# Optimization experiments

Measured on AMD Instinct MI355X. Metric: run time of the kernel, lower is better.

Reference implementation:

```python
import jax, jax.numpy as jnp
import numpy as np

B = 4096
IN_FEATS = 1024
OUT_FEATS = 1024
NUM_HEADS = 16
NUM_MEMS = 4096
HEAD_DIM = OUT_FEATS // NUM_HEADS
TEMPERATURE = 1.0
EPS = 0.0  # original code uses plain jnp.linalg.norm (no eps)


def setup_inputs() -> dict:
    key = jax.random.key(0)
    k1, k2, k3 = jax.random.split(key, 3)
    x = jax.random.normal(k1, (B, IN_FEATS), dtype=jnp.float32)
    # eqx.nn.Linear stores weight as [out, in]; uniform-like init replaced with normal scaled
    W_q = jax.random.normal(k2, (OUT_FEATS, IN_FEATS), dtype=jnp.float32) * (1.0 / np.sqrt(IN_FEATS))
    memories = jax.random.normal(k3, (NUM_HEADS, NUM_MEMS, HEAD_DIM), dtype=jnp.float32) * 0.02
    return {"x": x, "W_q": W_q, "memories": memories}


def reference(x, W_q, memories):
    # q = query_proj(x): [B, out_feats] -> [B, H, d]
    q = (x @ W_q.T).reshape(B, NUM_HEADS, HEAD_DIM)
    # L2-normalize queries and memories along feature dim
    q_norm = q / jnp.linalg.norm(q, axis=-1, keepdims=True)
    mem_norm = memories / jnp.linalg.norm(memories, axis=-1, keepdims=True)
    # cosine-similarity scores: [B, H, M]
    attn_scores = jnp.einsum('bhd,hmd->bhm', q_norm, mem_norm)
    # soft readout (hard=False branch)
    mem_probs = jax.nn.softmax(attn_scores / TEMPERATURE, axis=-1)
    # weighted combine of normalized memories, scaled by sqrt(head_dim)
    out = jnp.einsum('bhm,hmd->bhd', mem_probs, mem_norm) * jnp.sqrt(HEAD_DIM).astype(x.dtype)
    return out.reshape(B, OUT_FEATS)
```

## Files before the change

kernel.cpp:

```cpp
#include <hip/hip_runtime.h>
#include <stdint.h>

#define B_SZ  4096
#define HEADS 16
#define HD    64
#define M_SZ  4096
#define K_IN  1024
#define SW    72
#define LOG2E 1.44269504088896f

typedef _Float16 f16;
typedef f16  f16x4 __attribute__((ext_vector_type(4)));
typedef f16  f16x8 __attribute__((ext_vector_type(8)));
typedef float f32x4 __attribute__((ext_vector_type(4)));

union U8 { uint4 u4; f16x8 h8; unsigned int ui[4]; unsigned short us[8]; };

__device__ __forceinline__ unsigned short f2h(float f) {
    _Float16 h = (_Float16)f;
    return __builtin_bit_cast(unsigned short, h);
}
__device__ __forceinline__ f16x8 ldsv8(const unsigned short* p) {
    U8 u; u.u4 = *reinterpret_cast<const uint4*>(p); return u.h8;
}

#if __has_builtin(__builtin_amdgcn_exp2f)
#define EXP2F(x) __builtin_amdgcn_exp2f(x)
#else
#define EXP2F(x) __expf((x) * 0.6931471805599453f)
#endif

__device__ __forceinline__ void gload_lds16(const void* g, void* l) {
    __builtin_amdgcn_global_load_lds(
        (const __attribute__((address_space(1))) void*)g,
        (__attribute__((address_space(3))) void*)l, 16, 0, 0);
}

__global__ __launch_bounds__(256) void k_conv(const float* __restrict__ x,
                                              const float* __restrict__ Wq,
                                              unsigned short* __restrict__ xh,
                                              unsigned short* __restrict__ Wh) {
    const int b = blockIdx.x;
    const float* src;
    unsigned short* dst;
    size_t base;
    if (b < 2048) { src = x;  dst = xh; base = (size_t)b * 2048; }
    else          { src = Wq; dst = Wh; base = (size_t)(b - 2048) * 2048; }
    const size_t i = base + (size_t)threadIdx.x * 8;
    float4 f0 = reinterpret_cast<const float4*>(src + i)[0];
    float4 f1 = reinterpret_cast<const float4*>(src + i)[1];
    U8 u;
    u.us[0] = f2h(f0.x); u.us[1] = f2h(f0.y); u.us[2] = f2h(f0.z); u.us[3] = f2h(f0.w);
    u.us[4] = f2h(f1.x); u.us[5] = f2h(f1.y); u.us[6] = f2h(f1.z); u.us[7] = f2h(f1.w);
    *reinterpret_cast<uint4*>(dst + i) = u.u4;
}

__global__ __launch_bounds__(256) void k_prep_mem(const float* __restrict__ mem,
                                                  unsigned short* __restrict__ F) {
    __shared__ float part[64][4];
    __shared__ float scale[64];
    __shared__ unsigned short Tn[64 * SW];

    const int h  = blockIdx.y;
    const int tl = blockIdx.x;
    const int m0 = tl * 64;
    const int tid = threadIdx.x;
    const int r = tid >> 2;
    const int c = tid & 3;

    const float* src = mem + ((size_t)(h * M_SZ + m0 + r)) * HD + c * 16;
    float v[16];
    float ss = 0.f;
#pragma unroll
    for (int i = 0; i < 4; i++) {
        float4 f = reinterpret_cast<const float4*>(src)[i];
        v[4*i+0] = f.x; v[4*i+1] = f.y; v[4*i+2] = f.z; v[4*i+3] = f.w;
        ss += f.x*f.x + f.y*f.y + f.z*f.z + f.w*f.w;
    }
    part[r][c] = ss;
    __syncthreads();
    if (tid < 64) {
        float s = part[tid][0] + part[tid][1] + part[tid][2] + part[tid][3];
        scale[tid] = rsqrtf(s);
    }
    __syncthreads();
    const float sc = scale[r];

    U8 a, b;
#pragma unroll
    for (int i = 0; i < 8; i++) { a.us[i] = f2h(v[i] * sc); b.us[i] = f2h(v[8 + i] * sc); }
    *reinterpret_cast<uint4*>(&Tn[r * SW + c * 16])     = a.u4;
    *reinterpret_cast<uint4*>(&Tn[r * SW + c * 16 + 8]) = b.u4;
    __syncthreads();

    const int w = tid >> 6, lane = tid & 63;
    const int l15 = lane & 15, quad = lane >> 4;
    unsigned short* Fd = F + ((size_t)(h * 64 + tl) * 16) * 512;

#pragma unroll
    for (int i = 0; i < 2; i++) {
        const int ch = w * 2 + i, g = ch >> 1, s = ch & 1;
        const int mp = 32 * (g >> 1) + ((l15 >> 2) * 8) + 4 * (g & 1) + (l15 & 3);
        uint4 vv = *reinterpret_cast<const uint4*>(&Tn[mp * SW + s * 32 + quad * 8]);
        *reinterpret_cast<uint4*>(Fd + ch * 512 + lane * 8) = vv;
    }
#pragma unroll
    for (int i = 0; i < 2; i++) {
        const int c2 = w * 2 + i, p = c2 >> 2, n = c2 & 3;
        U8 u;
#pragma unroll
        for (int j = 0; j < 8; j++)
            u.us[j] = Tn[(32 * p + quad * 8 + j) * SW + n * 16 + l15];
        *reinterpret_cast<uint4*>(Fd + (8 + c2) * 512 + lane * 8) = u.u4;
    }
}

__global__ __launch_bounds__(256, 2) void k_qproj(const unsigned short* __restrict__ xh,
                                                  const unsigned short* __restrict__ Wh,
                                                  unsigned short* __restrict__ qn) {
    __shared__ unsigned short As[128 * SW];
    __shared__ unsigned short Bs[64 * SW];

    const int b0 = blockIdx.x * 128;
    const int n0 = blockIdx.y * 64;
    const int t = threadIdx.x;
    const int w = t >> 6, lane = t & 63;
    const int l15 = lane & 15, quad = lane >> 4;

    f32x4 acc[2][4] = {};

    for (int kb = 0; kb < K_IN; kb += 64) {
        __syncthreads();
        {
            const unsigned short* px = xh + (size_t)(b0 + (t >> 1)) * K_IN + kb + (t & 1) * 32;
            const unsigned short* pw = Wh + (size_t)(n0 + (t >> 2)) * K_IN + kb + (t & 3) * 16;
            uint4 av[4];
#pragma unroll
            for (int i = 0; i < 4; i++) av[i] = reinterpret_cast<const uint4*>(px)[i];
            uint4 bv[2];
#pragma unroll
            for (int i = 0; i < 2; i++) bv[i] = reinterpret_cast<const uint4*>(pw)[i];
#pragma unroll
            for (int i = 0; i < 4; i++)
                *reinterpret_cast<uint4*>(&As[(t >> 1) * SW + (t & 1) * 32 + i * 8]) = av[i];
#pragma unroll
            for (int i = 0; i < 2; i++)
                *reinterpret_cast<uint4*>(&Bs[(t >> 2) * SW + (t & 3) * 16 + i * 8]) = bv[i];
        }
        __syncthreads();

#pragma unroll
        for (int s = 0; s < 2; s++) {
            f16x8 af[2];
#pragma unroll
            for (int qg = 0; qg < 2; qg++)
                af[qg] = ldsv8(&As[(w * 32 + qg * 16 + l15) * SW + s * 32 + quad * 8]);
#pragma unroll
            for (int g = 0; g < 4; g++) {
                f16x8 bf_ = ldsv8(&Bs[(g * 16 + l15) * SW + s * 32 + quad * 8]);
#pragma unroll
                for (int qg = 0; qg < 2; qg++)
                    acc[qg][g] = __builtin_amdgcn_mfma_f32_16x16x32_f16(af[qg], bf_, acc[qg][g], 0, 0, 0);
            }
        }
    }

    __syncthreads();
    unsigned short* Ct = As;
#pragma unroll
    for (int qg = 0; qg < 2; qg++) {
        float ssq[4];
#pragma unroll
        for (int r = 0; r < 4; r++) {
            float s = 0.f;
#pragma unroll
            for (int g = 0; g < 4; g++) s += acc[qg][g][r] * acc[qg][g][r];
            ssq[r] = s;
        }
#pragma unroll
        for (int mask = 1; mask <= 8; mask <<= 1)
#pragma unroll
            for (int r = 0; r < 4; r++) ssq[r] += __shfl_xor(ssq[r], mask, 64);
#pragma unroll
        for (int r = 0; r < 4; r++) {
            float inv = rsqrtf(ssq[r]) * LOG2E;
#pragma unroll
            for (int g = 0; g < 4; g++)
                Ct[(w * 32 + qg * 16 + quad * 4 + r) * SW + g * 16 + l15] = f2h(acc[qg][g][r] * inv);
        }
    }
    __syncthreads();

    const int row = t >> 1, half = (t & 1) * 32;
    unsigned short* dq = qn + (size_t)(b0 + row) * 1024 + n0 + half;
#pragma unroll
    for (int i = 0; i < 4; i++)
        reinterpret_cast<uint4*>(dq)[i] = *reinterpret_cast<const uint4*>(&Ct[row * SW + half + i * 8]);
}

__global__ __launch_bounds__(256, 2) void k_attn(const unsigned short* __restrict__ qn,
                                                 const unsigned short* __restrict__ F,
                                                 float* __restrict__ out) {
    __shared__ unsigned short buf[2][8192];

    const int b = blockIdx.x;
    const int h  = 2 * (b & 7) + (b >> 8);
    const int b0 = ((b >> 3) & 31) * 128;
    const int t = threadIdx.x;
    const int w = t >> 6, lane = t & 63;
    const int l15 = lane & 15, quad = lane >> 4;

    f16x8 qf[2][2];
#pragma unroll
    for (int qg = 0; qg < 2; qg++)
#pragma unroll
        for (int s = 0; s < 2; s++) {
            U8 u;
            u.u4 = *reinterpret_cast<const uint4*>(
                qn + (size_t)(b0 + w * 32 + qg * 16 + l15) * 1024 + h * 64 + s * 32 + quad * 8);
            qf[qg][s] = u.h8;
        }

    const unsigned short* Fh = F + (size_t)h * 64 * 8192;

#pragma unroll
    for (int i = 0; i < 4; i++) {
        const int ch = w * 4 + i;
        gload_lds16(Fh + ch * 512 + lane * 8, &buf[0][ch * 512]);
    }

    f32x4 accO[2][4] = {};
    float lsum[2] = {0.f, 0.f};

    for (int tl = 0; tl < 64; ++tl) {
        __syncthreads();
        const int cur = tl & 1;

        if (tl + 1 < 64) {
            const unsigned short* gn = Fh + (size_t)(tl + 1) * 8192;
#pragma unroll
            for (int i = 0; i < 4; i++) {
                const int ch = w * 4 + i;
                gload_lds16(gn + ch * 512 + lane * 8, &buf[cur ^ 1][ch * 512]);
            }
        }

        const unsigned short* lb = buf[cur];
        f16x8 am[8], bw[8];
#pragma unroll
        for (int ch = 0; ch < 8; ch++) am[ch] = ldsv8(&lb[ch * 512 + lane * 8]);
#pragma unroll
        for (int ch = 0; ch < 8; ch++) bw[ch] = ldsv8(&lb[(8 + ch) * 512 + lane * 8]);

#pragma unroll
        for (int qg = 0; qg < 2; qg++) {
#pragma unroll
            for (int p = 0; p < 2; p++) {
                f32x4 s0 = {0.f, 0.f, 0.f, 0.f}, s1 = {0.f, 0.f, 0.f, 0.f};
                s0 = __builtin_amdgcn_mfma_f32_16x16x32_f16(am[4*p+0], qf[qg][0], s0, 0, 0, 0);
                s0 = __builtin_amdgcn_mfma_f32_16x16x32_f16(am[4*p+1], qf[qg][1], s0, 0, 0, 0);
                s1 = __builtin_amdgcn_mfma_f32_16x16x32_f16(am[4*p+2], qf[qg][0], s1, 0, 0, 0);
                s1 = __builtin_amdgcn_mfma_f32_16x16x32_f16(am[4*p+3], qf[qg][1], s1, 0, 0, 0);

                float p0 = EXP2F(s0[0]), p1 = EXP2F(s0[1]), p2 = EXP2F(s0[2]), p3 = EXP2F(s0[3]);
                float p4 = EXP2F(s1[0]), p5 = EXP2F(s1[1]), p6 = EXP2F(s1[2]), p7 = EXP2F(s1[3]);
                lsum[qg] += ((p0 + p1) + (p2 + p3)) + ((p4 + p5) + (p6 + p7));

                U8 pu;
#if __has_builtin(__builtin_amdgcn_cvt_pkrtz)
                pu.ui[0] = __builtin_bit_cast(unsigned int, __builtin_amdgcn_cvt_pkrtz(p0, p1));
                pu.ui[1] = __builtin_bit_cast(unsigned int, __builtin_amdgcn_cvt_pkrtz(p2, p3));
                pu.ui[2] = __builtin_bit_cast(unsigned int, __builtin_amdgcn_cvt_pkrtz(p4, p5));
                pu.ui[3] = __builtin_bit_cast(unsigned int, __builtin_amdgcn_cvt_pkrtz(p6, p7));
#else
                pu.us[0]=f2h(p0); pu.us[1]=f2h(p1); pu.us[2]=f2h(p2); pu.us[3]=f2h(p3);
                pu.us[4]=f2h(p4); pu.us[5]=f2h(p5); pu.us[6]=f2h(p6); pu.us[7]=f2h(p7);
#endif
#pragma unroll
                for (int n = 0; n < 4; n++)
                    accO[qg][n] = __builtin_amdgcn_mfma_f32_16x16x32_f16(pu.h8, bw[p * 4 + n], accO[qg][n], 0, 0, 0);
            }
        }
    }

#pragma unroll
    for (int qg = 0; qg < 2; qg++) {
        float s = lsum[qg];
        s += __shfl_xor(s, 16, 64);
        s += __shfl_xor(s, 32, 64);
        float inv = 8.0f / s;
#pragma unroll
        for (int r = 0; r < 4; r++) {
            float iv = __shfl(inv, quad * 4 + r, 64);
            float* po = out + (size_t)(b0 + w * 32 + qg * 16 + quad * 4 + r) * 1024 + h * 64;
#pragma unroll
            for (int n = 0; n < 4; n++)
                po[n * 16 + l15] = accO[qg][n][r] * iv;
        }
    }
}

extern "C" void kernel_launch(void* const* d_in, const int* in_sizes, int n_in,
                              void* d_out, int out_size, void* d_ws, size_t ws_size,
                              hipStream_t stream) {
    (void)in_sizes; (void)n_in; (void)out_size; (void)ws_size;
    const float* x   = (const float*)d_in[0];
    const float* Wq  = (const float*)d_in[1];
    const float* mem = (const float*)d_in[2];
    float* out = (float*)d_out;

    unsigned short* qn = (unsigned short*)d_ws;
    unsigned short* F  = qn + (size_t)B_SZ * 1024;
    unsigned short* xh = F  + (size_t)HEADS * 64 * 16 * 512;
    unsigned short* Wh = xh + (size_t)B_SZ * K_IN;

    k_conv    <<<2560, 256, 0, stream>>>(x, Wq, xh, Wh);
    k_prep_mem<<<dim3(64, 16), 256, 0, stream>>>(mem, F);
    k_qproj   <<<dim3(32, 16), 256, 0, stream>>>(xh, Wh, qn);
    k_attn    <<<512, 256, 0, stream>>>(qn, F, out);
}
```

Baseline: 179.1 us.

## Fuse fp32-to-fp16 conversion into q-projection GEMM and double attention tile size

Drops the separate conversion kernel: the q-projection now reads fp32 x and W_q directly and converts to fp16 while staging tiles into shared memory. The projection tile grows to 128x128 (two heads per block) with 256 blocks. The attention kernel now processes two memory tiles per iteration with a larger double buffer and a scheduling barrier. This removes one launch and the round-trip of fp16 copies through memory. In exchange it doubles the fp32 global reads per tile, gives less parallelism in the GEMM, and raises LDS and register pressure in the attention kernel, which may reduce occupancy.

```diff
diff --git a/kernel.cpp b/kernel.cpp
--- a/kernel.cpp
+++ b/kernel.cpp
@@ -30,29 +30,16 @@
 #define EXP2F(x) __expf((x) * 0.6931471805599453f)
 #endif
 
+#if __has_builtin(__builtin_amdgcn_sched_barrier)
+#define SCHED_FENCE() __builtin_amdgcn_sched_barrier(0)
+#else
+#define SCHED_FENCE()
+#endif
+
 __device__ __forceinline__ void gload_lds16(const void* g, void* l) {
     __builtin_amdgcn_global_load_lds(
         (const __attribute__((address_space(1))) void*)g,
         (__attribute__((address_space(3))) void*)l, 16, 0, 0);
-}
-
-__global__ __launch_bounds__(256) void k_conv(const float* __restrict__ x,
-                                              const float* __restrict__ Wq,
-                                              unsigned short* __restrict__ xh,
-                                              unsigned short* __restrict__ Wh) {
-    const int b = blockIdx.x;
-    const float* src;
-    unsigned short* dst;
-    size_t base;
-    if (b < 2048) { src = x;  dst = xh; base = (size_t)b * 2048; }
-    else          { src = Wq; dst = Wh; base = (size_t)(b - 2048) * 2048; }
-    const size_t i = base + (size_t)threadIdx.x * 8;
-    float4 f0 = reinterpret_cast<const float4*>(src + i)[0];
-    float4 f1 = reinterpret_cast<const float4*>(src + i)[1];
-    U8 u;
-    u.us[0] = f2h(f0.x); u.us[1] = f2h(f0.y); u.us[2] = f2h(f0.z); u.us[3] = f2h(f0.w);
-    u.us[4] = f2h(f1.x); u.us[5] = f2h(f1.y); u.us[6] = f2h(f1.z); u.us[7] = f2h(f1.w);
-    *reinterpret_cast<uint4*>(dst + i) = u.u4;
 }
 
 __global__ __launch_bounds__(256) void k_prep_mem(const float* __restrict__ mem,
@@ -115,37 +102,49 @@
     }
 }
 
-__global__ __launch_bounds__(256, 2) void k_qproj(const unsigned short* __restrict__ xh,
-                                                  const unsigned short* __restrict__ Wh,
-                                                  unsigned short* __restrict__ qn) {
-    __shared__ unsigned short As[128 * SW];
-    __shared__ unsigned short Bs[64 * SW];
-
-    const int b0 = blockIdx.x * 128;
-    const int n0 = blockIdx.y * 64;
+__global__ __launch_bounds__(256) void k_qproj(const float* __restrict__ x,
+                                               const float* __restrict__ Wq,
+                                               unsigned short* __restrict__ qn) {
+    __shared__ unsigned short sbuf[2 * 128 * SW];
+    unsigned short* As = sbuf;
+    unsigned short* Bs = sbuf + 128 * SW;
+
+    const int bx = blockIdx.x;
+    const int n0 = (bx & 7) * 128;
+    const int b0 = (bx >> 3) * 128;
     const int t = threadIdx.x;
     const int w = t >> 6, lane = t & 63;
     const int l15 = lane & 15, quad = lane >> 4;
 
-    f32x4 acc[2][4] = {};
-
+    f32x4 acc[2][8] = {};
+
+    const int sr = t >> 1, sk = (t & 1) * 32;
     for (int kb = 0; kb < K_IN; kb += 64) {
         __syncthreads();
         {
-            const unsigned short* px = xh + (size_t)(b0 + (t >> 1)) * K_IN + kb + (t & 1) * 32;
-            const unsigned short* pw = Wh + (size_t)(n0 + (t >> 2)) * K_IN + kb + (t & 3) * 16;
-            uint4 av[4];
-#pragma unroll
-            for (int i = 0; i < 4; i++) av[i] = reinterpret_cast<const uint4*>(px)[i];
-            uint4 bv[2];
-#pragma unroll
-            for (int i = 0; i < 2; i++) bv[i] = reinterpret_cast<const uint4*>(pw)[i];
-#pragma unroll
-            for (int i = 0; i < 4; i++)
-                *reinterpret_cast<uint4*>(&As[(t >> 1) * SW + (t & 1) * 32 + i * 8]) = av[i];
-#pragma unroll
-            for (int i = 0; i < 2; i++)
-                *reinterpret_cast<uint4*>(&Bs[(t >> 2) * SW + (t & 3) * 16 + i * 8]) = bv[i];
+            const float* px = x  + (size_t)(b0 + sr) * K_IN + kb + sk;
+            const float* pw = Wq + (size_t)(n0 + sr) * K_IN + kb + sk;
+            uint4 ox[4], ow[4];
+#pragma unroll
+            for (int i = 0; i < 4; i++) {
+                float4 f0 = reinterpret_cast<const float4*>(px)[2*i];
+                float4 f1 = reinterpret_cast<const float4*>(px)[2*i+1];
+                U8 u;
+                u.us[0]=f2h(f0.x); u.us[1]=f2h(f0.y); u.us[2]=f2h(f0.z); u.us[3]=f2h(f0.w);
+                u.us[4]=f2h(f1.x); u.us[5]=f2h(f1.y); u.us[6]=f2h(f1.z); u.us[7]=f2h(f1.w);
+                ox[i] = u.u4;
+                float4 g0 = reinterpret_cast<const float4*>(pw)[2*i];
+                float4 g1 = reinterpret_cast<const float4*>(pw)[2*i+1];
+                U8 v;
+                v.us[0]=f2h(g0.x); v.us[1]=f2h(g0.y); v.us[2]=f2h(g0.z); v.us[3]=f2h(g0.w);
+                v.us[4]=f2h(g1.x); v.us[5]=f2h(g1.y); v.us[6]=f2h(g1.z); v.us[7]=f2h(g1.w);
+                ow[i] = v.u4;
+            }
+#pragma unroll
+            for (int i = 0; i < 4; i++) {
+                *reinterpret_cast<uint4*>(&As[sr * SW + sk + i * 8]) = ox[i];
+                *reinterpret_cast<uint4*>(&Bs[sr * SW + sk + i * 8]) = ow[i];
+            }
         }
         __syncthreads();
 
@@ -156,7 +155,7 @@
             for (int qg = 0; qg < 2; qg++)
                 af[qg] = ldsv8(&As[(w * 32 + qg * 16 + l15) * SW + s * 32 + quad * 8]);
 #pragma unroll
-            for (int g = 0; g < 4; g++) {
+            for (int g = 0; g < 8; g++) {
                 f16x8 bf_ = ldsv8(&Bs[(g * 16 + l15) * SW + s * 32 + quad * 8]);
 #pragma unroll
                 for (int qg = 0; qg < 2; qg++)
@@ -166,42 +165,48 @@
     }
 
     __syncthreads();
-    unsigned short* Ct = As;
+    unsigned short* Ct = sbuf;
 #pragma unroll
     for (int qg = 0; qg < 2; qg++) {
-        float ssq[4];
+        float s0[4], s1[4];
 #pragma unroll
         for (int r = 0; r < 4; r++) {
-            float s = 0.f;
-#pragma unroll
-            for (int g = 0; g < 4; g++) s += acc[qg][g][r] * acc[qg][g][r];
-            ssq[r] = s;
+            float a = 0.f, b = 0.f;
+#pragma unroll
+            for (int g = 0; g < 4; g++) { a += acc[qg][g][r] * acc[qg][g][r];
+                                          b += acc[qg][g+4][r] * acc[qg][g+4][r]; }
+            s0[r] = a; s1[r] = b;
         }
 #pragma unroll
         for (int mask = 1; mask <= 8; mask <<= 1)
 #pragma unroll
-            for (int r = 0; r < 4; r++) ssq[r] += __shfl_xor(ssq[r], mask, 64);
+            for (int r = 0; r < 4; r++) { s0[r] += __shfl_xor(s0[r], mask, 64);
+                                          s1[r] += __shfl_xor(s1[r], mask, 64); }
 #pragma unroll
         for (int r = 0; r < 4; r++) {
-            float inv = rsqrtf(ssq[r]) * LOG2E;
-#pragma unroll
-            for (int g = 0; g < 4; g++)
-                Ct[(w * 32 + qg * 16 + quad * 4 + r) * SW + g * 16 + l15] = f2h(acc[qg][g][r] * inv);
-        }
-    }
-    __syncthreads();
-
-    const int row = t >> 1, half = (t & 1) * 32;
+            float i0 = rsqrtf(s0[r]) * LOG2E;
+            float i1 = rsqrtf(s1[r]) * LOG2E;
+            const int row = w * 32 + qg * 16 + quad * 4 + r;
+#pragma unroll
+            for (int g = 0; g < 4; g++) {
+                Ct[row * 136 + g * 16 + l15]      = f2h(acc[qg][g][r] * i0);
+                Ct[row * 136 + 64 + g * 16 + l15] = f2h(acc[qg][g+4][r] * i1);
+            }
+        }
+    }
+    __syncthreads();
+
+    const int row = t >> 1, half = (t & 1) * 64;
     unsigned short* dq = qn + (size_t)(b0 + row) * 1024 + n0 + half;
 #pragma unroll
-    for (int i = 0; i < 4; i++)
-        reinterpret_cast<uint4*>(dq)[i] = *reinterpret_cast<const uint4*>(&Ct[row * SW + half + i * 8]);
+    for (int i = 0; i < 8; i++)
+        reinterpret_cast<uint4*>(dq)[i] = *reinterpret_cast<const uint4*>(&Ct[row * 136 + half + i * 8]);
 }
 
 __global__ __launch_bounds__(256, 2) void k_attn(const unsigned short* __restrict__ qn,
                                                  const unsigned short* __restrict__ F,
                                                  float* __restrict__ out) {
-    __shared__ unsigned short buf[2][8192];
+    __shared__ unsigned short buf[2][16384];
 
     const int b = blockIdx.x;
     const int h  = 2 * (b & 7) + (b >> 8);
@@ -224,61 +229,70 @@
     const unsigned short* Fh = F + (size_t)h * 64 * 8192;
 
 #pragma unroll
-    for (int i = 0; i < 4; i++) {
-        const int ch = w * 4 + i;
+    for (int i = 0; i < 8; i++) {
+        const int ch = w * 8 + i;
         gload_lds16(Fh + ch * 512 + lane * 8, &buf[0][ch * 512]);
     }
 
     f32x4 accO[2][4] = {};
     float lsum[2] = {0.f, 0.f};
 
-    for (int tl = 0; tl < 64; ++tl) {
+    for (int it = 0; it < 32; ++it) {
         __syncthreads();
-        const int cur = tl & 1;
-
-        if (tl + 1 < 64) {
-            const unsigned short* gn = Fh + (size_t)(tl + 1) * 8192;
-#pragma unroll
-            for (int i = 0; i < 4; i++) {
-                const int ch = w * 4 + i;
+        const int cur = it & 1;
+
+        if (it + 1 < 32) {
+            const unsigned short* gn = Fh + (size_t)(it + 1) * 16384;
+#pragma unroll
+            for (int i = 0; i < 8; i++) {
+                const int ch = w * 8 + i;
                 gload_lds16(gn + ch * 512 + lane * 8, &buf[cur ^ 1][ch * 512]);
             }
         }
 
         const unsigned short* lb = buf[cur];
-        f16x8 am[8], bw[8];
-#pragma unroll
-        for (int ch = 0; ch < 8; ch++) am[ch] = ldsv8(&lb[ch * 512 + lane * 8]);
-#pragma unroll
-        for (int ch = 0; ch < 8; ch++) bw[ch] = ldsv8(&lb[(8 + ch) * 512 + lane * 8]);
-
-#pragma unroll
-        for (int qg = 0; qg < 2; qg++) {
-#pragma unroll
-            for (int p = 0; p < 2; p++) {
-                f32x4 s0 = {0.f, 0.f, 0.f, 0.f}, s1 = {0.f, 0.f, 0.f, 0.f};
-                s0 = __builtin_amdgcn_mfma_f32_16x16x32_f16(am[4*p+0], qf[qg][0], s0, 0, 0, 0);
-                s0 = __builtin_amdgcn_mfma_f32_16x16x32_f16(am[4*p+1], qf[qg][1], s0, 0, 0, 0);
-                s1 = __builtin_amdgcn_mfma_f32_16x16x32_f16(am[4*p+2], qf[qg][0], s1, 0, 0, 0);
-                s1 = __builtin_amdgcn_mfma_f32_16x16x32_f16(am[4*p+3], qf[qg][1], s1, 0, 0, 0);
-
-                float p0 = EXP2F(s0[0]), p1 = EXP2F(s0[1]), p2 = EXP2F(s0[2]), p3 = EXP2F(s0[3]);
-                float p4 = EXP2F(s1[0]), p5 = EXP2F(s1[1]), p6 = EXP2F(s1[2]), p7 = EXP2F(s1[3]);
-                lsum[qg] += ((p0 + p1) + (p2 + p3)) + ((p4 + p5) + (p6 + p7));
-
-                U8 pu;
+        f16x8 am[2][8], bw[2][8];
+#pragma unroll
+        for (int sub = 0; sub < 2; sub++) {
+#pragma unroll
+            for (int ch = 0; ch < 8; ch++)
+                am[sub][ch] = ldsv8(&lb[sub * 8192 + ch * 512 + lane * 8]);
+#pragma unroll
+            for (int ch = 0; ch < 8; ch++)
+                bw[sub][ch] = ldsv8(&lb[sub * 8192 + (8 + ch) * 512 + lane * 8]);
+        }
+        SCHED_FENCE();
+
+#pragma unroll
+        for (int sub = 0; sub < 2; sub++) {
+#pragma unroll
+            for (int qg = 0; qg < 2; qg++) {
+#pragma unroll
+                for (int p = 0; p < 2; p++) {
+                    f32x4 s0 = {0.f, 0.f, 0.f, 0.f}, s1 = {0.f, 0.f, 0.f, 0.f};
+                    s0 = __builtin_amdgcn_mfma_f32_16x16x32_f16(am[sub][4*p+0], qf[qg][0], s0, 0, 0, 0);
+                    s0 = __builtin_amdgcn_mfma_f32_16x16x32_f16(am[sub][4*p+1], qf[qg][1], s0, 0, 0, 0);
+                    s1 = __builtin_amdgcn_mfma_f32_16x16x32_f16(am[sub][4*p+2], qf[qg][0], s1, 0, 0, 0);
+                    s1 = __builtin_amdgcn_mfma_f32_16x16x32_f16(am[sub][4*p+3], qf[qg][1], s1, 0, 0, 0);
+
+                    float p0 = EXP2F(s0[0]), p1 = EXP2F(s0[1]), p2 = EXP2F(s0[2]), p3 = EXP2F(s0[3]);
+                    float p4 = EXP2F(s1[0]), p5 = EXP2F(s1[1]), p6 = EXP2F(s1[2]), p7 = EXP2F(s1[3]);
+                    lsum[qg] += ((p0 + p1) + (p2 + p3)) + ((p4 + p5) + (p6 + p7));
+
+                    U8 pu;
 #if __has_builtin(__builtin_amdgcn_cvt_pkrtz)
-                pu.ui[0] = __builtin_bit_cast(unsigned int, __builtin_amdgcn_cvt_pkrtz(p0, p1));
-                pu.ui[1] = __builtin_bit_cast(unsigned int, __builtin_amdgcn_cvt_pkrtz(p2, p3));
-                pu.ui[2] = __builtin_bit_cast(unsigned int, __builtin_amdgcn_cvt_pkrtz(p4, p5));
-                pu.ui[3] = __builtin_bit_cast(unsigned int, __builtin_amdgcn_cvt_pkrtz(p6, p7));
+                    pu.ui[0] = __builtin_bit_cast(unsigned int, __builtin_amdgcn_cvt_pkrtz(p0, p1));
+                    pu.ui[1] = __builtin_bit_cast(unsigned int, __builtin_amdgcn_cvt_pkrtz(p2, p3));
+                    pu.ui[2] = __builtin_bit_cast(unsigned int, __builtin_amdgcn_cvt_pkrtz(p4, p5));
+                    pu.ui[3] = __builtin_bit_cast(unsigned int, __builtin_amdgcn_cvt_pkrtz(p6, p7));
 #else
-                pu.us[0]=f2h(p0); pu.us[1]=f2h(p1); pu.us[2]=f2h(p2); pu.us[3]=f2h(p3);
-                pu.us[4]=f2h(p4); pu.us[5]=f2h(p5); pu.us[6]=f2h(p6); pu.us[7]=f2h(p7);
+                    pu.us[0]=f2h(p0); pu.us[1]=f2h(p1); pu.us[2]=f2h(p2); pu.us[3]=f2h(p3);
+                    pu.us[4]=f2h(p4); pu.us[5]=f2h(p5); pu.us[6]=f2h(p6); pu.us[7]=f2h(p7);
 #endif
 #pragma unroll
-                for (int n = 0; n < 4; n++)
-                    accO[qg][n] = __builtin_amdgcn_mfma_f32_16x16x32_f16(pu.h8, bw[p * 4 + n], accO[qg][n], 0, 0, 0);
+                    for (int n = 0; n < 4; n++)
+                        accO[qg][n] = __builtin_amdgcn_mfma_f32_16x16x32_f16(pu.h8, bw[sub][p * 4 + n], accO[qg][n], 0, 0, 0);
+                }
             }
         }
     }
@@ -311,11 +325,8 @@
 
     unsigned short* qn = (unsigned short*)d_ws;
     unsigned short* F  = qn + (size_t)B_SZ * 1024;
-    unsigned short* xh = F  + (size_t)HEADS * 64 * 16 * 512;
-    unsigned short* Wh = xh + (size_t)B_SZ * K_IN;
-
-    k_conv    <<<2560, 256, 0, stream>>>(x, Wq, xh, Wh);
+
     k_prep_mem<<<dim3(64, 16), 256, 0, stream>>>(mem, F);
-    k_qproj   <<<dim3(32, 16), 256, 0, stream>>>(xh, Wh, qn);
+    k_qproj   <<<256, 256, 0, stream>>>(x, Wq, qn);
     k_attn    <<<512, 256, 0, stream>>>(qn, F, out);
 }
```

New measurement: 206.6 us. 15.3% more time.
